# Kernel tuning notes

Hardware: AMD Instinct MI355X
Metric: run time of the kernel (lower is better)

The kernel has to match this reference:

```python
import jax, jax.numpy as jnp
import numpy as np


def setup_inputs() -> dict:
    key = jax.random.key(0)
    k1, k2, k3, k4 = jax.random.split(key, 4)
    N, E, IN, OUT = 100000, 1600000, 256, 32
    feat = jax.random.normal(k1, (N, IN), dtype=jnp.float32)
    src = jax.random.randint(k2, (E,), 0, N, dtype=jnp.int64)
    dst = jax.random.randint(k3, (E,), 0, N, dtype=jnp.int64)
    weight = jax.random.normal(k4, (IN, OUT), dtype=jnp.float32) * (6.0 / (IN + OUT)) ** 0.5
    bias = jnp.zeros((OUT,), dtype=jnp.float32)
    return {"feat": feat, "src": src, "dst": dst, "weight": weight, "bias": bias}


def reference(feat, src, dst, weight, bias):
    N = feat.shape[0]
    ones = jnp.ones(src.shape[0], dtype=feat.dtype)
    # norm='both': scale sources by out_degree^-0.5
    out_deg = jnp.clip(jax.ops.segment_sum(ones, src, num_segments=N), 1.0)
    feat = feat * (out_deg ** -0.5)[:, None]
    # in_feats (256) > out_feats (32): apply weight before aggregation
    feat = feat @ weight
    # SpMM: copy_src + sum over destination nodes
    rst = jax.ops.segment_sum(feat[src], dst, num_segments=N)  # [N, out]
    # scale destinations by in_degree^-0.5
    in_deg = jnp.clip(jax.ops.segment_sum(ones, dst, num_segments=N), 1.0)
    rst = rst * (in_deg ** -0.5)[:, None]
    rst = rst + bias
    return jax.nn.relu(rst)
```

## Files before the change

kernel.cpp:

```cpp
#include <hip/hip_runtime.h>
#include <hip/hip_bf16.h>


#define IN_F 256
#define OUT_F 32

#define G_ROWS 128
#define G_BK 16
#define W_ROWS 32
#define G_NT (IN_F / G_BK)

#define BSHIFT 7
#define BNODES 128
#define NBK 1024
#define PB_EDGES 4096
#define AGG_CAP 4096


__global__ __launch_bounds__(1024) void hist_kernel(
    const int* __restrict__ src, const int* __restrict__ dst,
    unsigned short* __restrict__ mhistS, unsigned short* __restrict__ mhistD,
    int E) {
  __shared__ int hS[NBK], hD[NBK];
  int tid = threadIdx.x;
  hS[tid] = 0; hD[tid] = 0;
  __syncthreads();
  int e0 = blockIdx.x * PB_EDGES + tid * 4;
  if (e0 + 4 <= E) {
    int4 a0 = *(const int4*)(src + e0);
    int4 b0 = *(const int4*)(dst + e0);
    int ss[4] = {a0.x, a0.y, a0.z, a0.w};
    int dd[4] = {b0.x, b0.y, b0.z, b0.w};
#pragma unroll
    for (int j = 0; j < 4; ++j) {
      atomicAdd(&hS[ss[j] >> BSHIFT], 1);
      atomicAdd(&hD[dd[j] >> BSHIFT], 1);
    }
  } else {
    for (int j = 0; j < 4; ++j) {
      int e = e0 + j;
      if (e < E) {
        atomicAdd(&hS[src[e] >> BSHIFT], 1);
        atomicAdd(&hD[dst[e] >> BSHIFT], 1);
      }
    }
  }
  __syncthreads();
  mhistS[blockIdx.x * NBK + tid] = (unsigned short)hS[tid];
  mhistD[blockIdx.x * NBK + tid] = (unsigned short)hD[tid];
}

__global__ __launch_bounds__(256) void offset_bucket_kernel(
    unsigned short* __restrict__ mhistS, unsigned short* __restrict__ mhistD,
    int* __restrict__ totS, int* __restrict__ totD, int npb) {
  int gid = blockIdx.x * 4 + (threadIdx.x >> 6);
  int lane = threadIdx.x & 63;
  int a = gid >> 10;
  int b = gid & (NBK - 1);
  unsigned short* mh = a ? mhistD : mhistS;
  int* tot = a ? totD : totS;
  int carry = 0;
  for (int c0 = 0; c0 < npb; c0 += 64) {
    int idx = c0 + lane;
    int v = (idx < npb) ? (int)mh[(size_t)idx * NBK + b] : 0;
    int x = v;
#pragma unroll
    for (int d = 1; d < 64; d <<= 1) {
      int y = __shfl_up(x, d, 64);
      if (lane >= d) x += y;
    }
    if (idx < npb) mh[(size_t)idx * NBK + b] = (unsigned short)(carry + x - v);
    carry += __shfl(x, 63, 64);
  }
  if (lane == 0) tot[b] = carry;
}

__global__ __launch_bounds__(1024) void offset_base_kernel(
    const int* __restrict__ totS, const int* __restrict__ totD,
    int* __restrict__ baseS, int* __restrict__ baseD) {
  __shared__ int wsum[16];
  const int* tt = blockIdx.x ? totD : totS;
  int* bb = blockIdx.x ? baseD : baseS;
  int b = threadIdx.x;
  int v = tt[b];
  int x = v;
#pragma unroll
  for (int d = 1; d < 64; d <<= 1) {
    int y = __shfl_up(x, d, 64);
    if ((b & 63) >= d) x += y;
  }
  if ((b & 63) == 63) wsum[b >> 6] = x;
  __syncthreads();
  int off = 0;
#pragma unroll
  for (int w = 0; w < 16; ++w)
    if (w < (b >> 6)) off += wsum[w];
  bb[b] = off + x - v;
  if (b == NBK - 1) bb[NBK] = off + x;
}

__global__ __launch_bounds__(1024) void partition_fused_kernel(
    const int* __restrict__ src, const int* __restrict__ dst,
    const unsigned short* __restrict__ mbaseS,
    const unsigned short* __restrict__ mbaseD,
    const int* __restrict__ baseS, const int* __restrict__ baseD,
    unsigned char* __restrict__ pairs_s, unsigned* __restrict__ pairs,
    int E, int npb) {
  __shared__ unsigned sbuf[PB_EDGES];
  __shared__ int hist[NBK];
  __shared__ int lbase[NBK + 1];
  __shared__ int gbase[NBK];
  __shared__ int wsum[16];

  int tid = threadIdx.x;
  bool isDst = (int)blockIdx.x >= npb;
  int pb = isDst ? (int)blockIdx.x - npb : (int)blockIdx.x;
  hist[tid] = 0;
  __syncthreads();

  int e0 = pb * PB_EDGES + tid * 4;
  int myb[4], myslot[4];
  unsigned mypk[4];
  unsigned char mylow[4];
  if (!isDst) {
    if (e0 + 4 <= E) {
      int4 a0 = *(const int4*)(src + e0);
      int ss[4] = {a0.x, a0.y, a0.z, a0.w};
#pragma unroll
      for (int j = 0; j < 4; ++j) {
        int b = ss[j] >> BSHIFT;
        myb[j] = b;
        mylow[j] = (unsigned char)(ss[j] & (BNODES - 1));
        myslot[j] = atomicAdd(&hist[b], 1);
      }
    } else {
#pragma unroll
      for (int j = 0; j < 4; ++j) {
        int e = e0 + j;
        if (e < E) {
          int s = src[e];
          int b = s >> BSHIFT;
          myb[j] = b;
          mylow[j] = (unsigned char)(s & (BNODES - 1));
          myslot[j] = atomicAdd(&hist[b], 1);
        } else {
          myb[j] = -1;
        }
      }
    }
  } else {
    if (e0 + 4 <= E) {
      int4 a0 = *(const int4*)(src + e0);
      int4 b0 = *(const int4*)(dst + e0);
      int ss[4] = {a0.x, a0.y, a0.z, a0.w};
      int dd[4] = {b0.x, b0.y, b0.z, b0.w};
#pragma unroll
      for (int j = 0; j < 4; ++j) {
        int b = dd[j] >> BSHIFT;
        myb[j] = b;
        mypk[j] = (unsigned)ss[j] | ((unsigned)(dd[j] & (BNODES - 1)) << 17);
        myslot[j] = atomicAdd(&hist[b], 1);
      }
    } else {
#pragma unroll
      for (int j = 0; j < 4; ++j) {
        int e = e0 + j;
        if (e < E) {
          int s = src[e], d = dst[e];
          int b = d >> BSHIFT;
          myb[j] = b;
          mypk[j] = (unsigned)s | ((unsigned)(d & (BNODES - 1)) << 17);
          myslot[j] = atomicAdd(&hist[b], 1);
        } else {
          myb[j] = -1;
        }
      }
    }
  }
  __syncthreads();

  {
    int v = hist[tid];
    int x = v;
#pragma unroll
    for (int d = 1; d < 64; d <<= 1) {
      int y = __shfl_up(x, d, 64);
      if ((tid & 63) >= d) x += y;
    }
    if ((tid & 63) == 63) wsum[tid >> 6] = x;
    __syncthreads();
    int off = 0;
#pragma unroll
    for (int w = 0; w < 16; ++w)
      if (w < (tid >> 6)) off += wsum[w];
    lbase[tid] = off + x - v;
    if (tid == NBK - 1) lbase[NBK] = off + x;
    if (isDst)
      gbase[tid] = baseD[tid] + (int)mbaseD[(size_t)pb * NBK + tid];
    else
      gbase[tid] = baseS[tid] + (int)mbaseS[(size_t)pb * NBK + tid];
  }
  __syncthreads();

  if (!isDst) {
    unsigned char* sbuf8 = (unsigned char*)sbuf;
#pragma unroll
    for (int j = 0; j < 4; ++j)
      if (myb[j] >= 0) sbuf8[lbase[myb[j]] + myslot[j]] = mylow[j];
  } else {
#pragma unroll
    for (int j = 0; j < 4; ++j)
      if (myb[j] >= 0) sbuf[lbase[myb[j]] + myslot[j]] = mypk[j];
  }
  __syncthreads();

  int total = lbase[NBK];
  int idx = tid * 4;
  if (idx < total) {
    int lo = 0, hi = NBK;
    while (hi - lo > 1) {
      int mid = (lo + hi) >> 1;
      if (lbase[mid] <= idx) lo = mid; else hi = mid;
    }
    int b = lo;
    if (!isDst) {
      unsigned char* sbuf8 = (unsigned char*)sbuf;
#pragma unroll
      for (int j = 0; j < 4; ++j, ++idx) {
        if (idx >= total) break;
        while (idx >= lbase[b + 1]) ++b;
        pairs_s[gbase[b] + (idx - lbase[b])] = sbuf8[idx];
      }
    } else {
#pragma unroll
      for (int j = 0; j < 4; ++j, ++idx) {
        if (idx >= total) break;
        while (idx >= lbase[b + 1]) ++b;
        pairs[gbase[b] + (idx - lbase[b])] = sbuf[idx];
      }
    }
  }
}

__global__ __launch_bounds__(256) void src_count_kernel(
    const unsigned char* __restrict__ pairs_s, const int* __restrict__ baseS,
    float* __restrict__ scale_out, int N) {
  __shared__ int hist[BNODES];
  int tid = threadIdx.x;
  int b = blockIdx.x;
  if (tid < BNODES) hist[tid] = 0;
  __syncthreads();
  int s = baseS[b], e = baseS[b + 1];
  for (int i = s + tid; i < e; i += 256) atomicAdd(&hist[pairs_s[i]], 1);
  __syncthreads();
  if (tid < BNODES) {
    int node = (b << BSHIFT) + tid;
    if (node < N) {
      int c = hist[tid];
      scale_out[node] = (c < 1) ? 1.f : rsqrtf((float)c);
    }
  }
}

__global__ __launch_bounds__(256, 4) void gemm_kernel(
    const float* __restrict__ feat, const float* __restrict__ W,
    const float* __restrict__ scale_out, float* __restrict__ h, int N) {
  __shared__ float sW[IN_F * OUT_F];
  __shared__ float sF[4][2][W_ROWS * G_BK];
  __shared__ float sScale[G_ROWS];

  int tid = threadIdx.x;
  int wv = tid >> 6;
  int lane = tid & 63;
  {
    const float4* W4 = (const float4*)W;
    float4* sW4 = (float4*)sW;
#pragma unroll
    for (int i = 0; i < 8; ++i) sW4[tid + i * 256] = W4[tid + i * 256];
  }
  int grow = blockIdx.x * G_ROWS;
  if (tid < G_ROWS) {
    int gr = grow + tid;
    sScale[tid] = (gr < N) ? scale_out[gr] : 0.f;
  }
  int wrow0 = grow + wv * W_ROWS;

  auto stage = [&](int t) {
    int k0 = t * G_BK;
    float* dstb = &sF[wv][t & 1][0];
#pragma unroll
    for (int q = 0; q < 2; ++q) {
      int r = q * 16 + (lane >> 2);
      int c = (lane & 3) ^ (r & 3);
      int g = wrow0 + r;
      if (g >= N) g = N - 1;
      const float* gp = feat + (size_t)g * IN_F + k0 + c * 4;
      __builtin_amdgcn_global_load_lds(
          (const __attribute__((address_space(1))) unsigned int*)gp,
          (__attribute__((address_space(3))) unsigned int*)(dstb + q * 256 + lane * 4),
          16, 0, 0);
    }
  };

  stage(0);

  int tr = lane >> 3;
  int cg = (lane & 7) * 4;

  float acc[4][4];
#pragma unroll
  for (int i = 0; i < 4; ++i)
#pragma unroll
    for (int c = 0; c < 4; ++c) acc[i][c] = 0.f;

  __syncthreads();

  for (int t = 0; t < G_NT; ++t) {
    if (t + 1 < G_NT) {
      stage(t + 1);
      asm volatile("s_waitcnt vmcnt(2)" ::: "memory");
    } else {
      asm volatile("s_waitcnt vmcnt(0)" ::: "memory");
    }

    const float* sf = &sF[wv][t & 1][0];
    int kb = t * G_BK;
#pragma unroll
    for (int cc = 0; cc < 4; ++cc) {
      float4 a[4];
#pragma unroll
      for (int i = 0; i < 4; ++i) {
        int r = tr + 8 * i;
        a[i] = *(const float4*)(sf + r * 16 + ((cc ^ (r & 3)) << 2));
      }
#pragma unroll
      for (int j = 0; j < 4; ++j) {
        float4 w = *(const float4*)(sW + (kb + cc * 4 + j) * OUT_F + cg);
#pragma unroll
        for (int i = 0; i < 4; ++i) {
          float aj = (j == 0) ? a[i].x : (j == 1) ? a[i].y
                   : (j == 2) ? a[i].z : a[i].w;
          acc[i][0] = fmaf(aj, w.x, acc[i][0]);
          acc[i][1] = fmaf(aj, w.y, acc[i][1]);
          acc[i][2] = fmaf(aj, w.z, acc[i][2]);
          acc[i][3] = fmaf(aj, w.w, acc[i][3]);
        }
      }
    }
  }

#pragma unroll
  for (int i = 0; i < 4; ++i) {
    int r = tr + 8 * i;
    int g = wrow0 + r;
    if (g < N) {
      float s = sScale[wv * W_ROWS + r];
      float4 o = {acc[i][0] * s, acc[i][1] * s, acc[i][2] * s, acc[i][3] * s};
      *(float4*)(h + (size_t)g * OUT_F + cg) = o;
    }
  }
}

__global__ __launch_bounds__(256) void sort_agg_kernel(
    const unsigned* __restrict__ pairs, const int* __restrict__ baseD,
    const float* __restrict__ h, const float* __restrict__ bias,
    float* __restrict__ out, int N) {
  __shared__ unsigned spk[AGG_CAP];
  __shared__ int hist[BNODES];
  __shared__ int rs[BNODES + 1];
  __shared__ int wsum2[4];

  int tid = threadIdx.x;
  int lane = tid & 31;
  int eg = tid >> 5;
  int b = blockIdx.x;
  int start = baseD[b];
  int end = baseD[b + 1];

  float acc[16];
  int degc[16];
#pragma unroll
  for (int t = 0; t < 16; ++t) { acc[t] = 0.f; degc[t] = 0; }

  for (int chunk = start; chunk < end; chunk += AGG_CAP) {
    int cnt = min(end - chunk, AGG_CAP);
    if (tid < BNODES) hist[tid] = 0;
    __syncthreads();

    unsigned mypk[16];
    int myslot[16];
    int nmine = 0;
    for (int i = tid; i < cnt; i += 256) {
      unsigned pk = pairs[chunk + i];
      mypk[nmine] = pk;
      myslot[nmine] = atomicAdd(&hist[pk >> 17], 1);
      ++nmine;
    }
    __syncthreads();

    {
      int v = (tid < BNODES) ? hist[tid] : 0;
      int x = v;
#pragma unroll
      for (int d = 1; d < 64; d <<= 1) {
        int y = __shfl_up(x, d, 64);
        if ((tid & 63) >= d) x += y;
      }
      if ((tid & 63) == 63) wsum2[tid >> 6] = x;
      __syncthreads();
      int off = (tid >= 64 && tid < BNODES) ? wsum2[0] : 0;
      if (tid < BNODES) rs[tid] = off + x - v;
      if (tid == BNODES - 1) rs[BNODES] = off + x;
    }
    __syncthreads();

    for (int i = 0; i < nmine; ++i) {
      unsigned pk = mypk[i];
      spk[rs[pk >> 17] + myslot[i]] = pk;
    }
    __syncthreads();

#pragma unroll 1
    for (int t = 0; t < 16; ++t) {
      int n = eg * 16 + t;
      int a = rs[n], bnd = rs[n + 1];
      degc[t] += bnd - a;
      float s = acc[t];
      int j = a;
      for (; j + 8 <= bnd; j += 8) {
        unsigned p0 = spk[j], p1 = spk[j + 1], p2 = spk[j + 2], p3 = spk[j + 3];
        unsigned p4 = spk[j + 4], p5 = spk[j + 5], p6 = spk[j + 6], p7 = spk[j + 7];
        float f0 = h[(size_t)(p0 & 0x1FFFF) * OUT_F + lane];
        float f1 = h[(size_t)(p1 & 0x1FFFF) * OUT_F + lane];
        float f2 = h[(size_t)(p2 & 0x1FFFF) * OUT_F + lane];
        float f3 = h[(size_t)(p3 & 0x1FFFF) * OUT_F + lane];
        float f4 = h[(size_t)(p4 & 0x1FFFF) * OUT_F + lane];
        float f5 = h[(size_t)(p5 & 0x1FFFF) * OUT_F + lane];
        float f6 = h[(size_t)(p6 & 0x1FFFF) * OUT_F + lane];
        float f7 = h[(size_t)(p7 & 0x1FFFF) * OUT_F + lane];
        s += ((f0 + f1) + (f2 + f3)) + ((f4 + f5) + (f6 + f7));
      }
      if (j + 4 <= bnd) {
        unsigned p0 = spk[j], p1 = spk[j + 1], p2 = spk[j + 2], p3 = spk[j + 3];
        float f0 = h[(size_t)(p0 & 0x1FFFF) * OUT_F + lane];
        float f1 = h[(size_t)(p1 & 0x1FFFF) * OUT_F + lane];
        float f2 = h[(size_t)(p2 & 0x1FFFF) * OUT_F + lane];
        float f3 = h[(size_t)(p3 & 0x1FFFF) * OUT_F + lane];
        s += (f0 + f1) + (f2 + f3);
        j += 4;
      }
      for (; j < bnd; ++j)
        s += h[(size_t)(spk[j] & 0x1FFFF) * OUT_F + lane];
      acc[t] = s;
    }
    __syncthreads();
  }

  int node0 = b << BSHIFT;
#pragma unroll
  for (int t = 0; t < 16; ++t) {
    int node = node0 + eg * 16 + t;
    if (node < N) {
      float sc = degc[t] > 0 ? rsqrtf((float)degc[t]) : 1.f;
      out[(size_t)node * OUT_F + lane] = fmaxf(fmaf(acc[t], sc, bias[lane]), 0.f);
    }
  }
}

__global__ __launch_bounds__(256) void degree_kernel(
    const int* __restrict__ src, const int* __restrict__ dst,
    int* __restrict__ cnt_out, int* __restrict__ cnt_in, int E) {
  int i = blockIdx.x * 256 + threadIdx.x;
  if (i < E) {
    atomicAdd(cnt_out + src[i], 1);
    atomicAdd(cnt_in + dst[i], 1);
  }
}

__global__ __launch_bounds__(256) void cnt_to_scale_kernel(
    const int* __restrict__ cnt, float* __restrict__ scale, int N) {
  int i = blockIdx.x * 256 + threadIdx.x;
  if (i < N) {
    int c = cnt[i];
    scale[i] = (c < 1) ? 1.f : rsqrtf((float)c);
  }
}

__global__ __launch_bounds__(256) void aggregate_kernel(
    const int* __restrict__ src, const int* __restrict__ dst,
    const float* __restrict__ h, float* __restrict__ out, int E) {
  int lane = threadIdx.x & 31;
  int e = (blockIdx.x * 256 + threadIdx.x) >> 5;
  if (e >= E) return;
  float v = h[(size_t)src[e] * OUT_F + lane];
  unsafeAtomicAdd(out + (size_t)dst[e] * OUT_F + lane, v);
}

__global__ __launch_bounds__(256) void finalize_kernel(
    float* __restrict__ out, const int* __restrict__ cnt_in,
    const float* __restrict__ bias, int N) {
  int idx = blockIdx.x * 256 + threadIdx.x;
  if (idx >= N * 8) return;
  int n = idx >> 3;
  int o = (idx & 7) * 4;
  float dg = (float)cnt_in[n];
  float s = dg < 1.f ? 1.f : rsqrtf(dg);
  float4 bv = *(const float4*)(bias + o);
  float4 v = ((const float4*)out)[idx];
  v.x = fmaxf(fmaf(v.x, s, bv.x), 0.f);
  v.y = fmaxf(fmaf(v.y, s, bv.y), 0.f);
  v.z = fmaxf(fmaf(v.z, s, bv.z), 0.f);
  v.w = fmaxf(fmaf(v.w, s, bv.w), 0.f);
  ((float4*)out)[idx] = v;
}

extern "C" void kernel_launch(void* const* d_in, const int* in_sizes, int n_in,
                              void* d_out, int out_size, void* d_ws, size_t ws_size,
                              hipStream_t stream) {
  const float* feat = (const float*)d_in[0];
  const int* src = (const int*)d_in[1];
  const int* dst = (const int*)d_in[2];
  const float* weight = (const float*)d_in[3];
  const float* bias = (const float*)d_in[4];
  float* out = (float*)d_out;

  int N = in_sizes[0] / IN_F;
  int E = in_sizes[1];
  int nb = (N + BNODES - 1) >> BSHIFT;
  int npb = (E + PB_EDGES - 1) / PB_EDGES;

  float* h = (float*)d_ws;
  unsigned* pairs = (unsigned*)(h + (size_t)N * OUT_F);
  unsigned char* pairs_s = (unsigned char*)pairs;
  pairs_s = (unsigned char*)(pairs + E);
  unsigned short* mhistS =
      (unsigned short*)(pairs_s + ((size_t)E + 3 & ~(size_t)3));
  unsigned short* mhistD = mhistS + (size_t)npb * NBK;
  int* baseS = (int*)(mhistD + (size_t)npb * NBK);
  int* baseD = baseS + NBK + 1;
  int* totS = baseD + NBK + 1;
  int* totD = totS + NBK;
  float* scale_out = (float*)(totD + NBK);

  size_t need = ((size_t)N * OUT_F + (size_t)E + (size_t)N +
                 2 * (NBK + 1) + 2 * NBK) * 4 +
                (size_t)E + (size_t)npb * NBK * 2 * 2 + 16;
  bool fast = (ws_size >= need) && (N <= (1 << 17)) && (nb <= NBK);

  if (fast) {
    hist_kernel<<<npb, 1024, 0, stream>>>(src, dst, mhistS, mhistD, E);
    offset_bucket_kernel<<<2 * NBK / 4, 256, 0, stream>>>(
        mhistS, mhistD, totS, totD, npb);
    offset_base_kernel<<<2, 1024, 0, stream>>>(totS, totD, baseS, baseD);
    partition_fused_kernel<<<2 * npb, 1024, 0, stream>>>(
        src, dst, mhistS, mhistD, baseS, baseD, pairs_s, pairs, E, npb);
    src_count_kernel<<<nb, 256, 0, stream>>>(pairs_s, baseS, scale_out, N);
    gemm_kernel<<<(N + G_ROWS - 1) / G_ROWS, 256, 0, stream>>>(
        feat, weight, scale_out, h, N);
    sort_agg_kernel<<<nb, 256, 0, stream>>>(pairs, baseD, h, bias, out, N);
  } else {
    int* cnt_out = (int*)(h + (size_t)N * OUT_F);
    int* cnt_in = cnt_out + N;
    float* scl = (float*)(cnt_in + N);
    hipMemsetAsync(cnt_out, 0, (size_t)2 * N * sizeof(int), stream);
    hipMemsetAsync(out, 0, (size_t)N * OUT_F * sizeof(float), stream);
    degree_kernel<<<(E + 255) / 256, 256, 0, stream>>>(src, dst, cnt_out, cnt_in, E);
    cnt_to_scale_kernel<<<(N + 255) / 256, 256, 0, stream>>>(cnt_out, scl, N);
    gemm_kernel<<<(N + G_ROWS - 1) / G_ROWS, 256, 0, stream>>>(feat, weight, scl, h, N);
    aggregate_kernel<<<(E + 7) / 8, 256, 0, stream>>>(src, dst, h, out, E);
    finalize_kernel<<<(N * 8 + 255) / 256, 256, 0, stream>>>(out, cnt_in, bias, N);
  }
}
```

Before: 272.5 us.

## Replace LDS-staged feature tiles in GEMM with direct global float4 loads

The feature-times-weight GEMM no longer stages feature tiles into shared memory through double-buffered async global-to-LDS loads. Each thread now reads its four rows straight from global memory as float4 pairs, eight K elements per step. The occupancy hint in launch bounds is dropped and shared-memory use shrinks to the weight and scale arrays, which may allow more resident blocks. The cost is that each row is read by eight lanes with poorly coalesced strided access, leaning on L1/L2 for reuse and losing the explicit prefetch overlap.

After: 284.7 us. 1.04x slower.

```diff
diff --git a/kernel.cpp b/kernel.cpp
--- a/kernel.cpp
+++ b/kernel.cpp
@@ -6,9 +6,6 @@
 #define OUT_F 32
 
 #define G_ROWS 128
-#define G_BK 16
-#define W_ROWS 32
-#define G_NT (IN_F / G_BK)
 
 #define BSHIFT 7
 #define BNODES 128
@@ -262,50 +259,34 @@
   }
 }
 
-__global__ __launch_bounds__(256, 4) void gemm_kernel(
+__global__ __launch_bounds__(256) void gemm_kernel(
     const float* __restrict__ feat, const float* __restrict__ W,
     const float* __restrict__ scale_out, float* __restrict__ h, int N) {
   __shared__ float sW[IN_F * OUT_F];
-  __shared__ float sF[4][2][W_ROWS * G_BK];
   __shared__ float sScale[G_ROWS];
 
   int tid = threadIdx.x;
-  int wv = tid >> 6;
-  int lane = tid & 63;
   {
     const float4* W4 = (const float4*)W;
     float4* sW4 = (float4*)sW;
 #pragma unroll
     for (int i = 0; i < 8; ++i) sW4[tid + i * 256] = W4[tid + i * 256];
   }
-  int grow = blockIdx.x * G_ROWS;
+  int row0 = blockIdx.x * G_ROWS;
   if (tid < G_ROWS) {
-    int gr = grow + tid;
+    int gr = row0 + tid;
     sScale[tid] = (gr < N) ? scale_out[gr] : 0.f;
   }
-  int wrow0 = grow + wv * W_ROWS;
-
-  auto stage = [&](int t) {
-    int k0 = t * G_BK;
-    float* dstb = &sF[wv][t & 1][0];
-#pragma unroll
-    for (int q = 0; q < 2; ++q) {
-      int r = q * 16 + (lane >> 2);
-      int c = (lane & 3) ^ (r & 3);
-      int g = wrow0 + r;
-      if (g >= N) g = N - 1;
-      const float* gp = feat + (size_t)g * IN_F + k0 + c * 4;
-      __builtin_amdgcn_global_load_lds(
-          (const __attribute__((address_space(1))) unsigned int*)gp,
-          (__attribute__((address_space(3))) unsigned int*)(dstb + q * 256 + lane * 4),
-          16, 0, 0);
-    }
-  };
-
-  stage(0);
-
-  int tr = lane >> 3;
-  int cg = (lane & 7) * 4;
+
+  int tr = tid >> 3;
+  int cg = (tid & 7) * 4;
+  const float4* fp[4];
+#pragma unroll
+  for (int i = 0; i < 4; ++i) {
+    int g = row0 + tr + 32 * i;
+    if (g >= N) g = N - 1;
+    fp[i] = (const float4*)(feat + (size_t)g * IN_F);
+  }
 
   float acc[4][4];
 #pragma unroll
@@ -315,46 +296,47 @@
 
   __syncthreads();
 
-  for (int t = 0; t < G_NT; ++t) {
-    if (t + 1 < G_NT) {
-      stage(t + 1);
-      asm volatile("s_waitcnt vmcnt(2)" ::: "memory");
-    } else {
-      asm volatile("s_waitcnt vmcnt(0)" ::: "memory");
-    }
-
-    const float* sf = &sF[wv][t & 1][0];
-    int kb = t * G_BK;
-#pragma unroll
-    for (int cc = 0; cc < 4; ++cc) {
-      float4 a[4];
+  for (int kb = 0; kb < IN_F; kb += 8) {
+    int kq = kb >> 2;
+    float4 a0[4], a1[4];
+#pragma unroll
+    for (int i = 0; i < 4; ++i) a0[i] = fp[i][kq];
+#pragma unroll
+    for (int i = 0; i < 4; ++i) a1[i] = fp[i][kq + 1];
+#pragma unroll
+    for (int j = 0; j < 4; ++j) {
+      float4 w = *(const float4*)(sW + (kb + j) * OUT_F + cg);
 #pragma unroll
       for (int i = 0; i < 4; ++i) {
-        int r = tr + 8 * i;
-        a[i] = *(const float4*)(sf + r * 16 + ((cc ^ (r & 3)) << 2));
-      }
-#pragma unroll
-      for (int j = 0; j < 4; ++j) {
-        float4 w = *(const float4*)(sW + (kb + cc * 4 + j) * OUT_F + cg);
-#pragma unroll
-        for (int i = 0; i < 4; ++i) {
-          float aj = (j == 0) ? a[i].x : (j == 1) ? a[i].y
-                   : (j == 2) ? a[i].z : a[i].w;
-          acc[i][0] = fmaf(aj, w.x, acc[i][0]);
-          acc[i][1] = fmaf(aj, w.y, acc[i][1]);
-          acc[i][2] = fmaf(aj, w.z, acc[i][2]);
-          acc[i][3] = fmaf(aj, w.w, acc[i][3]);
-        }
+        float aj = (j == 0) ? a0[i].x : (j == 1) ? a0[i].y
+                 : (j == 2) ? a0[i].z : a0[i].w;
+        acc[i][0] = fmaf(aj, w.x, acc[i][0]);
+        acc[i][1] = fmaf(aj, w.y, acc[i][1]);
+        acc[i][2] = fmaf(aj, w.z, acc[i][2]);
+        acc[i][3] = fmaf(aj, w.w, acc[i][3]);
+      }
+    }
+#pragma unroll
+    for (int j = 0; j < 4; ++j) {
+      float4 w = *(const float4*)(sW + (kb + 4 + j) * OUT_F + cg);
+#pragma unroll
+      for (int i = 0; i < 4; ++i) {
+        float aj = (j == 0) ? a1[i].x : (j == 1) ? a1[i].y
+                 : (j == 2) ? a1[i].z : a1[i].w;
+        acc[i][0] = fmaf(aj, w.x, acc[i][0]);
+        acc[i][1] = fmaf(aj, w.y, acc[i][1]);
+        acc[i][2] = fmaf(aj, w.z, acc[i][2]);
+        acc[i][3] = fmaf(aj, w.w, acc[i][3]);
       }
     }
   }
 
 #pragma unroll
   for (int i = 0; i < 4; ++i) {
-    int r = tr + 8 * i;
-    int g = wrow0 + r;
+    int r = tr + 32 * i;
+    int g = row0 + r;
     if (g < N) {
-      float s = sScale[wv * W_ROWS + r];
+      float s = sScale[r];
       float4 o = {acc[i][0] * s, acc[i][1] * s, acc[i][2] * s, acc[i][3] * s};
       *(float4*)(h + (size_t)g * OUT_F + cg) = o;
     }
@@ -531,8 +513,7 @@
 
   float* h = (float*)d_ws;
   unsigned* pairs = (unsigned*)(h + (size_t)N * OUT_F);
-  unsigned char* pairs_s = (unsigned char*)pairs;
-  pairs_s = (unsigned char*)(pairs + E);
+  unsigned char* pairs_s = (unsigned char*)(pairs + E);
   unsigned short* mhistS =
       (unsigned short*)(pairs_s + ((size_t)E + 3 & ~(size_t)3));
   unsigned short* mhistD = mhistS + (size_t)npb * NBK;
```
